# Performance work log

Hardware: AMD Instinct MI355X
Metric: run time of the kernel (lower is better)

Reference implementation:

```python
import jax, jax.numpy as jnp
import numpy as np

XN = 144
YN = 144
BN_EPS = 1e-5


def setup_inputs() -> dict:
    key = jax.random.key(0)
    k1, k2, k3, k4, k5 = jax.random.split(key, 5)
    B, P, M, F, C = 8, 12000, 32, 9, 64
    pillars = jax.random.normal(k1, (B, P, M, F), dtype=jnp.float32)
    pillar_indices = jax.random.randint(k2, (B, P, 3), 0, 144, dtype=jnp.int64)
    conv_w = jax.random.normal(k3, (C, F), dtype=jnp.float32) * 0.1  # 1x1 conv, no bias
    bn_gamma = jnp.ones((C,), dtype=jnp.float32)
    bn_beta = jnp.zeros((C,), dtype=jnp.float32)
    bn_mean = jax.random.normal(k4, (C,), dtype=jnp.float32) * 0.01
    bn_var = jax.random.uniform(k5, (C,), dtype=jnp.float32, minval=0.5, maxval=1.5)
    return {"pillars": pillars, "pillar_indices": pillar_indices, "conv_w": conv_w,
            "bn_gamma": bn_gamma, "bn_beta": bn_beta, "bn_mean": bn_mean, "bn_var": bn_var}


def reference(pillars, pillar_indices, conv_w, bn_gamma, bn_beta, bn_mean, bn_var):
    # pillars: [B, P, M, F] -> 1x1 conv over feature dim -> [B, C, P, M]
    x = jnp.einsum('bpmf,cf->bcpm', pillars, conv_w)
    # BatchNorm2d (inference) + ReLU
    inv_std = jax.lax.rsqrt(bn_var + BN_EPS)
    x = (x - bn_mean[None, :, None, None]) * (bn_gamma * inv_std)[None, :, None, None] \
        + bn_beta[None, :, None, None]
    x = jax.nn.relu(x)
    # MaxPool2d((1, M)): max over points-per-pillar axis -> [B, C, P]
    feat = jnp.max(x, axis=-1)
    # Scatter pillar features into BEV canvas [C, Xn*Yn]
    y_idx = pillar_indices[:, :, 1]                      # [B, P]
    x_idx = jnp.clip(pillar_indices[:, :, 2], 0, 143)    # [B, P]
    flat_idx = y_idx * XN + x_idx                        # [B, P]

    C = feat.shape[1]

    def scatter_one(f, idx):  # f: [C, P], idx: [P]
        canvas = jnp.zeros((C, XN * YN), dtype=f.dtype)
        return canvas.at[:, idx].set(f)

    out = jax.vmap(scatter_one)(feat, flat_idx)          # [B, C, Xn*Yn]
    return out.reshape(feat.shape[0], C, XN, YN)
```

## Files before the change

kernel.cpp:

```cpp
#include <hip/hip_runtime.h>
#include <hip/hip_bf16.h>
#include <stdint.h>

#define NB 8
#define NP 12000
#define NM 32
#define NF 9
#define NC 64
#define NX 144
#define NCELL (144*144)

#define PCHUNK 16
#define NCHUNK ((NB*NP)/PCHUNK)

typedef __attribute__((ext_vector_type(8)))  short bfrag8;
typedef __attribute__((ext_vector_type(16))) float accf16;

#define WS_BTAB  0
#define WS_SHIFT 2048
#define WS_WIN   4096
#define WS_FEAT  668672
#define WS_NEED  (WS_FEAT + (size_t)NB*NP*NC*4)

__global__ void winner_prep_kernel(const int* __restrict__ idx, int* __restrict__ winner,
                                   const float* __restrict__ conv_w,
                                   const float* __restrict__ gamma,
                                   const float* __restrict__ beta,
                                   const float* __restrict__ mean,
                                   const float* __restrict__ var,
                                   unsigned short* __restrict__ btab,
                                   float* __restrict__ shift)
{
    int t = blockIdx.x * blockDim.x + threadIdx.x;
    if (t < NB * NP) {
        int b = t / NP;
        int p = t - b * NP;
        int y = idx[t * 3 + 1];
        int x = idx[t * 3 + 2];
        x = x < 0 ? 0 : (x > 143 ? 143 : x);
        y = y < 0 ? 0 : (y > 143 ? 143 : y);
        atomicMax(&winner[b * NCELL + y * NX + x], p);
    }
    if (blockIdx.x == 0) {
        int tt = threadIdx.x;
        if (tt < 128) {
            int ct = tt >> 6, L = tt & 63;
            int c  = ct * 32 + (L & 31);
            int kq = L >> 5;
            float sc = gamma[c] * rsqrtf(var[c] + 1e-5f);
            unsigned short* dst = btab + (ct * 64 + L) * 8;
            #pragma unroll
            for (int j = 0; j < 8; ++j) {
                int k = kq * 8 + j;
                float w = (k < NF) ? conv_w[c * NF + k] * sc : 0.f;
                __hip_bfloat16 h = __float2bfloat16(w);
                dst[j] = *(unsigned short*)&h;
            }
        }
        if (tt < NC) {
            float sc = gamma[tt] * rsqrtf(var[tt] + 1e-5f);
            shift[tt] = beta[tt] - mean[tt] * sc;
        }
    }
}

template <bool COMPACT>
__global__ void __launch_bounds__(256) feat_mfma_kernel(
    const float* __restrict__ pillars,
    const int*   __restrict__ idx,
    const unsigned short* __restrict__ btab,
    const float* __restrict__ shift,
    const int*   __restrict__ winner,
    float* __restrict__ feat_ws,
    float* __restrict__ out)
{
    __shared__ unsigned short tile[PCHUNK * NM * 16];
    int tid  = threadIdx.x;
    int lane = tid & 63;
    int wave = tid >> 6;
    int chunk = blockIdx.x;

    #pragma unroll
    for (int rr = 0; rr < 2; ++rr) {
        int r = tid + rr * 256;
        tile[r * 16 + 9] = 0;
        *(unsigned int*)&tile[r * 16 + 10] = 0;
        *(unsigned int*)&tile[r * 16 + 12] = 0;
        *(unsigned int*)&tile[r * 16 + 14] = 0;
    }
    const float2* src = (const float2*)(pillars + (long long)chunk * (PCHUNK * NM * NF));
    #pragma unroll
    for (int i = 0; i < 9; ++i) {
        int le2 = tid + i * 256;
        float2 v = src[le2];
        int le = le2 * 2;
        int r = le / 9;
        int f = le - r * 9;
        __hip_bfloat16 hx = __float2bfloat16(v.x);
        tile[r * 16 + f] = *(unsigned short*)&hx;
        int f2 = f + 1, r2 = r;
        if (f2 == 9) { f2 = 0; r2 = r + 1; }
        __hip_bfloat16 hy = __float2bfloat16(v.y);
        tile[r2 * 16 + f2] = *(unsigned short*)&hy;
    }
    __syncthreads();

    bfrag8 b0 = *(const bfrag8*)(btab + lane * 8);
    bfrag8 b1 = *(const bfrag8*)(btab + (64 + lane) * 8);
    float  sh = shift[lane];

    int row = lane & 31;
    int kq  = lane >> 5;

    #pragma unroll
    for (int i = 0; i < 4; ++i) {
        int pr  = wave * 4 + i;
        int pil = chunk * PCHUNK + pr;
        int b   = pil / NP;
        int p   = pil - b * NP;
        int y = idx[pil * 3 + 1];
        int x = idx[pil * 3 + 2];
        x = x < 0 ? 0 : (x > 143 ? 143 : x);
        y = y < 0 ? 0 : (y > 143 ? 143 : y);
        int cell = y * NX + x;
        if (winner[b * NCELL + cell] != p) continue;

        bfrag8 a = *(const bfrag8*)&tile[pr * 512 + row * 16 + kq * 8];
        accf16 z = (accf16)0.0f;
        accf16 acc0 = __builtin_amdgcn_mfma_f32_32x32x16_bf16(a, b0, z, 0, 0, 0);
        accf16 acc1 = __builtin_amdgcn_mfma_f32_32x32x16_bf16(a, b1, z, 0, 0, 0);

        float v0 = acc0[0], v1 = acc1[0];
        #pragma unroll
        for (int j = 1; j < 16; ++j) { v0 = fmaxf(v0, acc0[j]); v1 = fmaxf(v1, acc1[j]); }
        v0 = fmaxf(v0, __shfl_xor(v0, 32));
        v1 = fmaxf(v1, __shfl_xor(v1, 32));
        float r = (lane < 32) ? v0 : v1;
        r = r + sh;
        r = r > 0.f ? r : 0.f;

        if (COMPACT) {
            feat_ws[(long long)pil * NC + lane] = r;
        } else {
            out[((long long)(b * NC + lane)) * NCELL + cell] = r;
        }
    }
}

__global__ void scatter_kernel(const int* __restrict__ winner,
                               const float* __restrict__ feat_ws,
                               float* __restrict__ out)
{
    int t = blockIdx.x * blockDim.x + threadIdx.x;
    if (t >= NB * (NCELL / 4)) return;
    int b  = t / (NCELL / 4);
    int c4 = t - b * (NCELL / 4);
    int cellbase = c4 * 4;

    int4 wv = *(const int4*)(winner + b * NCELL + cellbase);
    long long base0 = wv.x < 0 ? -1 : ((long long)(b * NP + wv.x)) * NC;
    long long base1 = wv.y < 0 ? -1 : ((long long)(b * NP + wv.y)) * NC;
    long long base2 = wv.z < 0 ? -1 : ((long long)(b * NP + wv.z)) * NC;
    long long base3 = wv.w < 0 ? -1 : ((long long)(b * NP + wv.w)) * NC;

    const float4 z = make_float4(0.f, 0.f, 0.f, 0.f);
    #pragma unroll 4
    for (int c0 = 0; c0 < NC; c0 += 4) {
        float4 f0 = base0 < 0 ? z : *(const float4*)(feat_ws + base0 + c0);
        float4 f1 = base1 < 0 ? z : *(const float4*)(feat_ws + base1 + c0);
        float4 f2 = base2 < 0 ? z : *(const float4*)(feat_ws + base2 + c0);
        float4 f3 = base3 < 0 ? z : *(const float4*)(feat_ws + base3 + c0);
        float* o = out + ((long long)(b * NC + c0)) * NCELL + cellbase;
        *(float4*)(o + 0LL * NCELL) = make_float4(f0.x, f1.x, f2.x, f3.x);
        *(float4*)(o + 1LL * NCELL) = make_float4(f0.y, f1.y, f2.y, f3.y);
        *(float4*)(o + 2LL * NCELL) = make_float4(f0.z, f1.z, f2.z, f3.z);
        *(float4*)(o + 3LL * NCELL) = make_float4(f0.w, f1.w, f2.w, f3.w);
    }
}

extern "C" void kernel_launch(void* const* d_in, const int* in_sizes, int n_in,
                              void* d_out, int out_size, void* d_ws, size_t ws_size,
                              hipStream_t stream) {
    const float* pillars = (const float*)d_in[0];
    const int*   idx     = (const int*)d_in[1];
    const float* conv_w  = (const float*)d_in[2];
    const float* gamma   = (const float*)d_in[3];
    const float* beta    = (const float*)d_in[4];
    const float* mean    = (const float*)d_in[5];
    const float* var     = (const float*)d_in[6];
    float* out = (float*)d_out;

    char* ws = (char*)d_ws;
    unsigned short* btab  = (unsigned short*)(ws + WS_BTAB);
    float*          shift = (float*)(ws + WS_SHIFT);
    int*            winner = (int*)(ws + WS_WIN);
    float*          feat_ws = (float*)(ws + WS_FEAT);

    const bool compact = ws_size >= WS_NEED;

    hipMemsetAsync(winner, 0xFF, (size_t)NB * NCELL * sizeof(int), stream);
    winner_prep_kernel<<<(NB * NP + 255) / 256, 256, 0, stream>>>(
        idx, winner, conv_w, gamma, beta, mean, var, btab, shift);

    if (compact) {
        feat_mfma_kernel<true><<<NCHUNK, 256, 0, stream>>>(
            pillars, idx, btab, shift, winner, feat_ws, out);
        scatter_kernel<<<(NB * (NCELL / 4) + 255) / 256, 256, 0, stream>>>(
            winner, feat_ws, out);
    } else {
        hipMemsetAsync(out, 0, (size_t)out_size * sizeof(float), stream);
        feat_mfma_kernel<false><<<NCHUNK, 256, 0, stream>>>(
            pillars, idx, btab, shift, winner, feat_ws, out);
    }
}
```

Measured before the change: 211.0 us.

## Load pillars directly into MFMA fragments and split scatter across channel quarters

The feature kernel drops the shared-memory bf16 staging tile and barrier. Each wave now loads its pillar rows from global memory straight into MFMA A-fragments and processes 8 pillars. In compact mode it computes features for every pillar without the winner check, so work on losing pillars is no longer skipped. The scatter kernel splits the 64 channels into four quarters handled by separate threads, raising parallelism for the canvas writes. Per-lane row loads are strided by 9 floats, which may coalesce worse than the previous float2 staging.

Result: no change. 210.1 us (-0.4%).

```diff
diff --git a/kernel.cpp b/kernel.cpp
--- a/kernel.cpp
+++ b/kernel.cpp
@@ -10,8 +10,9 @@
 #define NX 144
 #define NCELL (144*144)
 
-#define PCHUNK 16
-#define NCHUNK ((NB*NP)/PCHUNK)
+#define PPW 8
+#define FEAT_WAVES ((NB*NP)/PPW)
+#define FEAT_BLOCKS (FEAT_WAVES/4)
 
 typedef __attribute__((ext_vector_type(8)))  short bfrag8;
 typedef __attribute__((ext_vector_type(16))) float accf16;
@@ -65,68 +66,40 @@
 }
 
 template <bool COMPACT>
-__global__ void __launch_bounds__(256) feat_mfma_kernel(
+__global__ void __launch_bounds__(256) feat_dense_kernel(
     const float* __restrict__ pillars,
-    const int*   __restrict__ idx,
     const unsigned short* __restrict__ btab,
     const float* __restrict__ shift,
+    const int*   __restrict__ idx,
     const int*   __restrict__ winner,
     float* __restrict__ feat_ws,
     float* __restrict__ out)
 {
-    __shared__ unsigned short tile[PCHUNK * NM * 16];
     int tid  = threadIdx.x;
     int lane = tid & 63;
-    int wave = tid >> 6;
-    int chunk = blockIdx.x;
-
-    #pragma unroll
-    for (int rr = 0; rr < 2; ++rr) {
-        int r = tid + rr * 256;
-        tile[r * 16 + 9] = 0;
-        *(unsigned int*)&tile[r * 16 + 10] = 0;
-        *(unsigned int*)&tile[r * 16 + 12] = 0;
-        *(unsigned int*)&tile[r * 16 + 14] = 0;
-    }
-    const float2* src = (const float2*)(pillars + (long long)chunk * (PCHUNK * NM * NF));
-    #pragma unroll
-    for (int i = 0; i < 9; ++i) {
-        int le2 = tid + i * 256;
-        float2 v = src[le2];
-        int le = le2 * 2;
-        int r = le / 9;
-        int f = le - r * 9;
-        __hip_bfloat16 hx = __float2bfloat16(v.x);
-        tile[r * 16 + f] = *(unsigned short*)&hx;
-        int f2 = f + 1, r2 = r;
-        if (f2 == 9) { f2 = 0; r2 = r + 1; }
-        __hip_bfloat16 hy = __float2bfloat16(v.y);
-        tile[r2 * 16 + f2] = *(unsigned short*)&hy;
-    }
-    __syncthreads();
+    int wave = blockIdx.x * 4 + (tid >> 6);
+    int row  = lane & 31;
+    int kq   = lane >> 5;
 
     bfrag8 b0 = *(const bfrag8*)(btab + lane * 8);
     bfrag8 b1 = *(const bfrag8*)(btab + (64 + lane) * 8);
     float  sh = shift[lane];
+    accf16 z  = {};
 
-    int row = lane & 31;
-    int kq  = lane >> 5;
-
-    #pragma unroll
-    for (int i = 0; i < 4; ++i) {
-        int pr  = wave * 4 + i;
-        int pil = chunk * PCHUNK + pr;
-        int b   = pil / NP;
-        int p   = pil - b * NP;
-        int y = idx[pil * 3 + 1];
-        int x = idx[pil * 3 + 2];
-        x = x < 0 ? 0 : (x > 143 ? 143 : x);
-        y = y < 0 ? 0 : (y > 143 ? 143 : y);
-        int cell = y * NX + x;
-        if (winner[b * NCELL + cell] != p) continue;
-
-        bfrag8 a = *(const bfrag8*)&tile[pr * 512 + row * 16 + kq * 8];
-        accf16 z = (accf16)0.0f;
+    #pragma unroll 2
+    for (int i = 0; i < PPW; ++i) {
+        int pil = wave * PPW + i;
+        const float* base = pillars + (size_t)pil * (NM * NF) + row * NF;
+        float f[9];
+        #pragma unroll
+        for (int j = 0; j < 9; ++j) f[j] = base[j];
+        bfrag8 a;
+        #pragma unroll
+        for (int j = 0; j < 8; ++j) {
+            float g = kq ? (j == 0 ? f[8] : 0.f) : f[j];
+            __hip_bfloat16 h = __float2bfloat16(g);
+            a[j] = *(short*)&h;
+        }
         accf16 acc0 = __builtin_amdgcn_mfma_f32_32x32x16_bf16(a, b0, z, 0, 0, 0);
         accf16 acc1 = __builtin_amdgcn_mfma_f32_32x32x16_bf16(a, b1, z, 0, 0, 0);
 
@@ -136,25 +109,33 @@
         v0 = fmaxf(v0, __shfl_xor(v0, 32));
         v1 = fmaxf(v1, __shfl_xor(v1, 32));
         float r = (lane < 32) ? v0 : v1;
-        r = r + sh;
+        r += sh;
         r = r > 0.f ? r : 0.f;
 
         if (COMPACT) {
-            feat_ws[(long long)pil * NC + lane] = r;
+            feat_ws[(size_t)pil * NC + lane] = r;
         } else {
-            out[((long long)(b * NC + lane)) * NCELL + cell] = r;
+            int b = pil / NP, p = pil - b * NP;
+            int y = idx[pil * 3 + 1], x = idx[pil * 3 + 2];
+            x = x < 0 ? 0 : (x > 143 ? 143 : x);
+            y = y < 0 ? 0 : (y > 143 ? 143 : y);
+            int cell = y * NX + x;
+            if (winner[b * NCELL + cell] == p)
+                out[((size_t)(b * NC + lane)) * NCELL + cell] = r;
         }
     }
 }
 
-__global__ void scatter_kernel(const int* __restrict__ winner,
-                               const float* __restrict__ feat_ws,
-                               float* __restrict__ out)
+__global__ void __launch_bounds__(256) scatter_kernel(
+    const int* __restrict__ winner,
+    const float* __restrict__ feat_ws,
+    float* __restrict__ out)
 {
-    int t = blockIdx.x * blockDim.x + threadIdx.x;
-    if (t >= NB * (NCELL / 4)) return;
-    int b  = t / (NCELL / 4);
-    int c4 = t - b * (NCELL / 4);
+    int t  = blockIdx.x * blockDim.x + threadIdx.x;
+    int c4 = t % (NCELL / 4);
+    int bq = t / (NCELL / 4);
+    int q  = bq & 3;
+    int b  = bq >> 2;
     int cellbase = c4 * 4;
 
     int4 wv = *(const int4*)(winner + b * NCELL + cellbase);
@@ -163,18 +144,19 @@
     long long base2 = wv.z < 0 ? -1 : ((long long)(b * NP + wv.z)) * NC;
     long long base3 = wv.w < 0 ? -1 : ((long long)(b * NP + wv.w)) * NC;
 
-    const float4 z = make_float4(0.f, 0.f, 0.f, 0.f);
-    #pragma unroll 4
-    for (int c0 = 0; c0 < NC; c0 += 4) {
-        float4 f0 = base0 < 0 ? z : *(const float4*)(feat_ws + base0 + c0);
-        float4 f1 = base1 < 0 ? z : *(const float4*)(feat_ws + base1 + c0);
-        float4 f2 = base2 < 0 ? z : *(const float4*)(feat_ws + base2 + c0);
-        float4 f3 = base3 < 0 ? z : *(const float4*)(feat_ws + base3 + c0);
-        float* o = out + ((long long)(b * NC + c0)) * NCELL + cellbase;
-        *(float4*)(o + 0LL * NCELL) = make_float4(f0.x, f1.x, f2.x, f3.x);
-        *(float4*)(o + 1LL * NCELL) = make_float4(f0.y, f1.y, f2.y, f3.y);
-        *(float4*)(o + 2LL * NCELL) = make_float4(f0.z, f1.z, f2.z, f3.z);
-        *(float4*)(o + 3LL * NCELL) = make_float4(f0.w, f1.w, f2.w, f3.w);
+    const float4 zf = make_float4(0.f, 0.f, 0.f, 0.f);
+    #pragma unroll
+    for (int k = 0; k < 4; ++k) {
+        int c0 = q * 16 + k * 4;
+        float4 f0 = base0 < 0 ? zf : *(const float4*)(feat_ws + base0 + c0);
+        float4 f1 = base1 < 0 ? zf : *(const float4*)(feat_ws + base1 + c0);
+        float4 f2 = base2 < 0 ? zf : *(const float4*)(feat_ws + base2 + c0);
+        float4 f3 = base3 < 0 ? zf : *(const float4*)(feat_ws + base3 + c0);
+        float* o = out + ((size_t)(b * NC + c0)) * NCELL + cellbase;
+        *(float4*)(o + 0ULL * NCELL) = make_float4(f0.x, f1.x, f2.x, f3.x);
+        *(float4*)(o + 1ULL * NCELL) = make_float4(f0.y, f1.y, f2.y, f3.y);
+        *(float4*)(o + 2ULL * NCELL) = make_float4(f0.z, f1.z, f2.z, f3.z);
+        *(float4*)(o + 3ULL * NCELL) = make_float4(f0.w, f1.w, f2.w, f3.w);
     }
 }
 
@@ -191,9 +173,9 @@
     float* out = (float*)d_out;
 
     char* ws = (char*)d_ws;
-    unsigned short* btab  = (unsigned short*)(ws + WS_BTAB);
-    float*          shift = (float*)(ws + WS_SHIFT);
-    int*            winner = (int*)(ws + WS_WIN);
+    unsigned short* btab    = (unsigned short*)(ws + WS_BTAB);
+    float*          shift   = (float*)(ws + WS_SHIFT);
+    int*            winner  = (int*)(ws + WS_WIN);
     float*          feat_ws = (float*)(ws + WS_FEAT);
 
     const bool compact = ws_size >= WS_NEED;
@@ -203,13 +185,13 @@
         idx, winner, conv_w, gamma, beta, mean, var, btab, shift);
 
     if (compact) {
-        feat_mfma_kernel<true><<<NCHUNK, 256, 0, stream>>>(
-            pillars, idx, btab, shift, winner, feat_ws, out);
-        scatter_kernel<<<(NB * (NCELL / 4) + 255) / 256, 256, 0, stream>>>(
-            winner, feat_ws, out);
+        feat_dense_kernel<true><<<FEAT_BLOCKS, 256, 0, stream>>>(
+            pillars, btab, shift, idx, winner, feat_ws, out);
+        int sthreads = NB * 4 * (NCELL / 4);
+        scatter_kernel<<<sthreads / 256, 256, 0, stream>>>(winner, feat_ws, out);
     } else {
         hipMemsetAsync(out, 0, (size_t)out_size * sizeof(float), stream);
-        feat_mfma_kernel<false><<<NCHUNK, 256, 0, stream>>>(
-            pillars, idx, btab, shift, winner, feat_ws, out);
+        feat_dense_kernel<false><<<FEAT_BLOCKS, 256, 0, stream>>>(
+            pillars, btab, shift, idx, winner, feat_ws, out);
     }
 }
```
